# Kernel optimization log

Measured on AMD Instinct MI355X. Metric: run time of the kernel, lower is better.

Reference implementation:

```python
import jax, jax.numpy as jnp
import numpy as np
from jax import lax

D_MODEL = 1024
D_STATE = 16
BATCH = 4
SEQ = 2048
EPS = 1e-5


def setup_inputs() -> dict:
    key = jax.random.key(0)
    ks = jax.random.split(key, 5)
    x = jax.random.normal(ks[0], (BATCH, SEQ, D_MODEL), dtype=jnp.float32)
    A_log = jax.random.normal(ks[1], (D_MODEL, D_STATE), dtype=jnp.float32) * 0.1
    # nn.Linear default init ~ U(-1/sqrt(fan_in), 1/sqrt(fan_in))
    B_w = jax.random.uniform(ks[2], (D_STATE, D_MODEL), minval=-1.0, maxval=1.0) / np.sqrt(D_MODEL)
    C_w = jax.random.uniform(ks[3], (D_MODEL, D_STATE), minval=-1.0, maxval=1.0) / np.sqrt(D_STATE)
    D = jnp.ones((D_MODEL,), dtype=jnp.float32)
    gamma = jnp.ones((D_MODEL,), dtype=jnp.float32)
    beta = jnp.zeros((D_MODEL,), dtype=jnp.float32)
    return {"x": x, "A_log": A_log, "B_w": B_w, "C_w": C_w, "D": D, "gamma": gamma, "beta": beta}


def _layernorm(y, gamma, beta):
    mu = jnp.mean(y, axis=-1, keepdims=True)
    var = jnp.mean((y - mu) ** 2, axis=-1, keepdims=True)
    return (y - mu) * lax.rsqrt(var + EPS) * gamma + beta


def reference(x, A_log, B_w, C_w, D, gamma, beta):
    batch, seq_len, d = x.shape
    decay = jnp.exp(-jnp.exp(A_log))  # (d_model, d_state), exp(A) with A = -exp(A_log)
    # Precompute all B projections: (batch, seq, d_state)
    bx = jnp.einsum('bsd,nd->bsn', x, B_w)
    bx_t = jnp.swapaxes(bx, 0, 1)  # (seq, batch, d_state)

    def step(h, b_t):
        # h: (batch, d_model, d_state); b_t broadcast over d_model dim
        h = h * decay + b_t[:, None, :]
        return h, h.mean(axis=1)  # carry, per-step mean (batch, d_state)

    h0 = jnp.zeros((batch, d, A_log.shape[1]), dtype=x.dtype)
    _, hmeans = lax.scan(step, h0, bx_t)  # hmeans: (seq, batch, d_state)

    y = jnp.einsum('sbn,dn->bsd', hmeans, C_w) + D * x  # (batch, seq, d_model)
    return _layernorm(y, gamma, beta)
```

## Files before the change

kernel.cpp:

```cpp
#include <hip/hip_runtime.h>
#include <hip/hip_bf16.h>

#define D_MODEL 1024
#define D_STATE 16
#define BATCH   4
#define SEQ     2048
#define ROWS    (BATCH*SEQ)
#define WIN     64

#define K1_ROWS 8
__global__ __launch_bounds__(256, 4) void k_proj(const float* __restrict__ x,
                                                 const float* __restrict__ Bw,
                                                 const float* __restrict__ A_log,
                                                 float* __restrict__ bx,
                                                 float* __restrict__ KbarT) {
    __shared__ float xs[K1_ROWS][1024];
    __shared__ float red[4][8][K1_ROWS][2];
    const int tid = threadIdx.x;

    if (blockIdx.x >= ROWS / K1_ROWS) {
        const int n = blockIdx.x - ROWS / K1_ROWS;
        float* l2   = &xs[0][0];
        float* kred = &xs[1][0];
        const int delta = tid & 63;
        const int c     = tid >> 6;
        for (int d = tid; d < D_MODEL; d += 256) {
            float a = A_log[d * D_STATE + n];
            l2[d] = -expf(a) * 1.4426950408889634f;
        }
        __syncthreads();
        const float fdelta = (float)delta;
        float acc = 0.f;
        const int d0 = c * 256;
        for (int d = d0; d < d0 + 256; ++d)
            acc += exp2f(fdelta * l2[d]);
        kred[c * WIN + delta] = acc;
        __syncthreads();
        if (tid < WIN)
            KbarT[tid * D_STATE + n] =
                (kred[tid] + kred[WIN + tid] + kred[2 * WIN + tid] + kred[3 * WIN + tid])
                * (1.0f / 1024.0f);
        return;
    }

    const int np   = tid & 7;
    const int dblk = tid >> 3;
    const int row0 = blockIdx.x * K1_ROWS;
    const int lane = tid & 63, wid = tid >> 6;

    float4 bw0[8], bw1[8];
    {
        const float4* p0 = reinterpret_cast<const float4*>(Bw + (size_t)(2 * np    ) * 1024 + dblk * 32);
        const float4* p1 = reinterpret_cast<const float4*>(Bw + (size_t)(2 * np + 1) * 1024 + dblk * 32);
#pragma unroll
        for (int j = 0; j < 8; ++j) { bw0[j] = p0[j]; bw1[j] = p1[j]; }
    }

    const int chunk = tid >> 3;
    const int slotw = ((tid & 7) + chunk) & 7;
#pragma unroll
    for (int r = 0; r < K1_ROWS; ++r) {
        float4 v = reinterpret_cast<const float4*>(x + (size_t)(row0 + r) * 1024)[tid];
        *reinterpret_cast<float4*>(&xs[r][chunk * 32 + slotw * 4]) = v;
    }
    __syncthreads();

    float a0[K1_ROWS], a1[K1_ROWS];
#pragma unroll
    for (int r = 0; r < K1_ROWS; ++r) { a0[r] = 0.f; a1[r] = 0.f; }

#pragma unroll
    for (int r = 0; r < K1_ROWS; ++r) {
#pragma unroll
        for (int j = 0; j < 8; ++j) {
            const int slot = (j + dblk) & 7;
            float4 xv = *reinterpret_cast<const float4*>(&xs[r][dblk * 32 + slot * 4]);
            a0[r] = fmaf(xv.x, bw0[j].x, a0[r]); a0[r] = fmaf(xv.y, bw0[j].y, a0[r]);
            a0[r] = fmaf(xv.z, bw0[j].z, a0[r]); a0[r] = fmaf(xv.w, bw0[j].w, a0[r]);
            a1[r] = fmaf(xv.x, bw1[j].x, a1[r]); a1[r] = fmaf(xv.y, bw1[j].y, a1[r]);
            a1[r] = fmaf(xv.z, bw1[j].z, a1[r]); a1[r] = fmaf(xv.w, bw1[j].w, a1[r]);
        }
    }

#pragma unroll
    for (int r = 0; r < K1_ROWS; ++r) {
        float v0 = a0[r], v1 = a1[r];
        v0 += __shfl_xor(v0, 8);  v1 += __shfl_xor(v1, 8);
        v0 += __shfl_xor(v0, 16); v1 += __shfl_xor(v1, 16);
        v0 += __shfl_xor(v0, 32); v1 += __shfl_xor(v1, 32);
        a0[r] = v0; a1[r] = v1;
    }
    if (lane < 8) {
#pragma unroll
        for (int r = 0; r < K1_ROWS; ++r) {
            red[wid][lane][r][0] = a0[r];
            red[wid][lane][r][1] = a1[r];
        }
    }
    __syncthreads();
    if (tid < K1_ROWS * 16) {
        const int r = tid >> 4, n = tid & 15;
        float v = red[0][n >> 1][r][n & 1] + red[1][n >> 1][r][n & 1]
                + red[2][n >> 1][r][n & 1] + red[3][n >> 1][r][n & 1];
        bx[(size_t)(row0 + r) * D_STATE + n] = v;
    }
}

#define KO_ROWS 8
__global__ __launch_bounds__(256, 4) void k_tail(const float* __restrict__ x,
                                                 const float* __restrict__ bxg,
                                                 const float* __restrict__ KbarT,
                                                 const float* __restrict__ Cw,
                                                 const float* __restrict__ Dp,
                                                 const float* __restrict__ gamma,
                                                 const float* __restrict__ beta,
                                                 float* __restrict__ out) {
    const int tid = threadIdx.x;
    const int row0 = blockIdx.x * KO_ROWS;
    const int lane = tid & 63, wid = tid >> 6;
    __shared__ float4 bwin[71][4];
    __shared__ float4 kb4[WIN][4];
    __shared__ float4 hm4[KO_ROWS][4];
    __shared__ float red_s[2][4][4], red_q[2][4][4];

    kb4[tid >> 2][tid & 3] = reinterpret_cast<const float4*>(KbarT)[tid];
    const float4* bx4 = reinterpret_cast<const float4*>(bxg);
    for (int f = tid; f < 71 * 4; f += 256) {
        const int j = f >> 2, q = f & 3;
        long g = (long)row0 - 63 + j;
        if (g < 0) g = 0;
        bwin[j][q] = bx4[g * 4 + q];
    }
    __syncthreads();

    {
        const int r_f = tid >> 5, dc = (tid >> 2) & 7, nq = tid & 3;
        const int t0 = row0 & (SEQ - 1);
        float4 acc = {0.f, 0.f, 0.f, 0.f};
        if (t0 >= WIN) {
#pragma unroll
            for (int j = 0; j < 8; ++j) {
                const int delta = dc * 8 + j;
                const float4 b = bwin[63 + r_f - delta][nq];
                const float4 k = kb4[delta][nq];
                acc.x = fmaf(k.x, b.x, acc.x); acc.y = fmaf(k.y, b.y, acc.y);
                acc.z = fmaf(k.z, b.z, acc.z); acc.w = fmaf(k.w, b.w, acc.w);
            }
        } else {
            const int t = t0 + r_f;
#pragma unroll
            for (int j = 0; j < 8; ++j) {
                const int delta = dc * 8 + j;
                if (delta <= t) {
                    const float4 b = bwin[63 + r_f - delta][nq];
                    const float4 k = kb4[delta][nq];
                    acc.x = fmaf(k.x, b.x, acc.x); acc.y = fmaf(k.y, b.y, acc.y);
                    acc.z = fmaf(k.z, b.z, acc.z); acc.w = fmaf(k.w, b.w, acc.w);
                }
            }
        }
#pragma unroll
        for (int off = 4; off <= 16; off <<= 1) {
            acc.x += __shfl_xor(acc.x, off);
            acc.y += __shfl_xor(acc.y, off);
            acc.z += __shfl_xor(acc.z, off);
            acc.w += __shfl_xor(acc.w, off);
        }
        if (dc == 0) hm4[r_f][nq] = acc;
    }
    __syncthreads();

    float4 cw[4][4];
#pragma unroll
    for (int j = 0; j < 4; ++j) {
        const float4* p = reinterpret_cast<const float4*>(Cw + (size_t)(tid * 4 + j) * D_STATE);
#pragma unroll
        for (int q = 0; q < 4; ++q) cw[j][q] = p[q];
    }
    const float4 Dq = reinterpret_cast<const float4*>(Dp)[tid];
    const float4 gq = reinterpret_cast<const float4*>(gamma)[tid];
    const float4 bq = reinterpret_cast<const float4*>(beta)[tid];

    for (int h = 0; h < 2; ++h) {
        float4 y[4];
#pragma unroll
        for (int rr = 0; rr < 4; ++rr) {
            const int r = h * 4 + rr;
            const size_t row = row0 + r;
            const float4 h0 = hm4[r][0], h1 = hm4[r][1], h2 = hm4[r][2], h3 = hm4[r][3];
            const float4 xq = reinterpret_cast<const float4*>(x + row * D_MODEL)[tid];

            float4 v;
#pragma unroll
            for (int j = 0; j < 4; ++j) {
                float a = 0.f;
                a = fmaf(h0.x, cw[j][0].x, a); a = fmaf(h0.y, cw[j][0].y, a);
                a = fmaf(h0.z, cw[j][0].z, a); a = fmaf(h0.w, cw[j][0].w, a);
                a = fmaf(h1.x, cw[j][1].x, a); a = fmaf(h1.y, cw[j][1].y, a);
                a = fmaf(h1.z, cw[j][1].z, a); a = fmaf(h1.w, cw[j][1].w, a);
                a = fmaf(h2.x, cw[j][2].x, a); a = fmaf(h2.y, cw[j][2].y, a);
                a = fmaf(h2.z, cw[j][2].z, a); a = fmaf(h2.w, cw[j][2].w, a);
                a = fmaf(h3.x, cw[j][3].x, a); a = fmaf(h3.y, cw[j][3].y, a);
                a = fmaf(h3.z, cw[j][3].z, a); a = fmaf(h3.w, cw[j][3].w, a);
                ((float*)&v)[j] = a;
            }
            v.x = fmaf(Dq.x, xq.x, v.x);
            v.y = fmaf(Dq.y, xq.y, v.y);
            v.z = fmaf(Dq.z, xq.z, v.z);
            v.w = fmaf(Dq.w, xq.w, v.w);
            y[rr] = v;

            float s  = v.x + v.y + v.z + v.w;
            float sq = v.x*v.x + v.y*v.y + v.z*v.z + v.w*v.w;
            s += __shfl_xor(s, 1);  sq += __shfl_xor(sq, 1);
            s += __shfl_xor(s, 2);  sq += __shfl_xor(sq, 2);
            s += __shfl_xor(s, 4);  sq += __shfl_xor(sq, 4);
            s += __shfl_xor(s, 8);  sq += __shfl_xor(sq, 8);
            s += __shfl_xor(s, 16); sq += __shfl_xor(sq, 16);
            s += __shfl_xor(s, 32); sq += __shfl_xor(sq, 32);
            if (lane == 0) { red_s[h][rr][wid] = s; red_q[h][rr][wid] = sq; }
        }
        __syncthreads();

#pragma unroll
        for (int rr = 0; rr < 4; ++rr) {
            const int r = h * 4 + rr;
            const size_t row = row0 + r;
            const float ssum = red_s[h][rr][0] + red_s[h][rr][1] + red_s[h][rr][2] + red_s[h][rr][3];
            const float ssq  = red_q[h][rr][0] + red_q[h][rr][1] + red_q[h][rr][2] + red_q[h][rr][3];
            const float mu   = ssum * (1.0f / 1024.0f);
            const float var  = ssq * (1.0f / 1024.0f) - mu * mu;
            const float inv  = rsqrtf(var + 1e-5f);
            const float4 v = y[rr];
            float4 o;
            o.x = fmaf((v.x - mu) * inv, gq.x, bq.x);
            o.y = fmaf((v.y - mu) * inv, gq.y, bq.y);
            o.z = fmaf((v.z - mu) * inv, gq.z, bq.z);
            o.w = fmaf((v.w - mu) * inv, gq.w, bq.w);
            reinterpret_cast<float4*>(out + row * D_MODEL)[tid] = o;
        }
    }
}

extern "C" void kernel_launch(void* const* d_in, const int* in_sizes, int n_in,
                              void* d_out, int out_size, void* d_ws, size_t ws_size,
                              hipStream_t stream) {
    (void)in_sizes; (void)n_in; (void)out_size; (void)ws_size;
    const float* x     = (const float*)d_in[0];
    const float* A_log = (const float*)d_in[1];
    const float* B_w   = (const float*)d_in[2];
    const float* C_w   = (const float*)d_in[3];
    const float* Dp    = (const float*)d_in[4];
    const float* gamma = (const float*)d_in[5];
    const float* beta  = (const float*)d_in[6];
    float* out = (float*)d_out;

    float* bx = (float*)d_ws;
    float* kb = bx + (size_t)ROWS * D_STATE;

    k_proj<<<ROWS / K1_ROWS + D_STATE, 256, 0, stream>>>(x, B_w, A_log, bx, kb);
    k_tail<<<ROWS / KO_ROWS,           256, 0, stream>>>(x, bx, kb, C_w, Dp, gamma, beta, out);
}
```

Before: 56.83 us.

## Prefetch x rows early in tail kernel and schedule decay blocks first

The tail kernel now issues all eight x-row loads at kernel start, so their latency overlaps the bx window staging and the hidden-mean computation. The two half-row passes are merged into one pass with a single barrier. Launch bounds drop to 3 waves per SIMD to make room for the extra registers. In the projection kernel the 16 decay-kernel blocks move to the front of the grid so the long exp-sum blocks start first instead of trailing at the end.

```diff
diff --git a/kernel.cpp b/kernel.cpp
--- a/kernel.cpp
+++ b/kernel.cpp
@@ -18,8 +18,8 @@
     __shared__ float red[4][8][K1_ROWS][2];
     const int tid = threadIdx.x;
 
-    if (blockIdx.x >= ROWS / K1_ROWS) {
-        const int n = blockIdx.x - ROWS / K1_ROWS;
+    if (blockIdx.x < D_STATE) {
+        const int n = blockIdx.x;
         float* l2   = &xs[0][0];
         float* kred = &xs[1][0];
         const int delta = tid & 63;
@@ -45,7 +45,7 @@
 
     const int np   = tid & 7;
     const int dblk = tid >> 3;
-    const int row0 = blockIdx.x * K1_ROWS;
+    const int row0 = (blockIdx.x - D_STATE) * K1_ROWS;
     const int lane = tid & 63, wid = tid >> 6;
 
     float4 bw0[8], bw1[8];
@@ -107,7 +107,7 @@
 }
 
 #define KO_ROWS 8
-__global__ __launch_bounds__(256, 4) void k_tail(const float* __restrict__ x,
+__global__ __launch_bounds__(256, 3) void k_tail(const float* __restrict__ x,
                                                  const float* __restrict__ bxg,
                                                  const float* __restrict__ KbarT,
                                                  const float* __restrict__ Cw,
@@ -121,7 +121,12 @@
     __shared__ float4 bwin[71][4];
     __shared__ float4 kb4[WIN][4];
     __shared__ float4 hm4[KO_ROWS][4];
-    __shared__ float red_s[2][4][4], red_q[2][4][4];
+    __shared__ float red_s[KO_ROWS][4], red_q[KO_ROWS][4];
+
+    float4 xq[KO_ROWS];
+#pragma unroll
+    for (int r = 0; r < KO_ROWS; ++r)
+        xq[r] = reinterpret_cast<const float4*>(x + (size_t)(row0 + r) * D_MODEL)[tid];
 
     kb4[tid >> 2][tid & 3] = reinterpret_cast<const float4*>(KbarT)[tid];
     const float4* bx4 = reinterpret_cast<const float4*>(bxg);
@@ -181,64 +186,57 @@
     const float4 gq = reinterpret_cast<const float4*>(gamma)[tid];
     const float4 bq = reinterpret_cast<const float4*>(beta)[tid];
 
-    for (int h = 0; h < 2; ++h) {
-        float4 y[4];
-#pragma unroll
-        for (int rr = 0; rr < 4; ++rr) {
-            const int r = h * 4 + rr;
-            const size_t row = row0 + r;
-            const float4 h0 = hm4[r][0], h1 = hm4[r][1], h2 = hm4[r][2], h3 = hm4[r][3];
-            const float4 xq = reinterpret_cast<const float4*>(x + row * D_MODEL)[tid];
-
-            float4 v;
-#pragma unroll
-            for (int j = 0; j < 4; ++j) {
-                float a = 0.f;
-                a = fmaf(h0.x, cw[j][0].x, a); a = fmaf(h0.y, cw[j][0].y, a);
-                a = fmaf(h0.z, cw[j][0].z, a); a = fmaf(h0.w, cw[j][0].w, a);
-                a = fmaf(h1.x, cw[j][1].x, a); a = fmaf(h1.y, cw[j][1].y, a);
-                a = fmaf(h1.z, cw[j][1].z, a); a = fmaf(h1.w, cw[j][1].w, a);
-                a = fmaf(h2.x, cw[j][2].x, a); a = fmaf(h2.y, cw[j][2].y, a);
-                a = fmaf(h2.z, cw[j][2].z, a); a = fmaf(h2.w, cw[j][2].w, a);
-                a = fmaf(h3.x, cw[j][3].x, a); a = fmaf(h3.y, cw[j][3].y, a);
-                a = fmaf(h3.z, cw[j][3].z, a); a = fmaf(h3.w, cw[j][3].w, a);
-                ((float*)&v)[j] = a;
-            }
-            v.x = fmaf(Dq.x, xq.x, v.x);
-            v.y = fmaf(Dq.y, xq.y, v.y);
-            v.z = fmaf(Dq.z, xq.z, v.z);
-            v.w = fmaf(Dq.w, xq.w, v.w);
-            y[rr] = v;
-
-            float s  = v.x + v.y + v.z + v.w;
-            float sq = v.x*v.x + v.y*v.y + v.z*v.z + v.w*v.w;
-            s += __shfl_xor(s, 1);  sq += __shfl_xor(sq, 1);
-            s += __shfl_xor(s, 2);  sq += __shfl_xor(sq, 2);
-            s += __shfl_xor(s, 4);  sq += __shfl_xor(sq, 4);
-            s += __shfl_xor(s, 8);  sq += __shfl_xor(sq, 8);
-            s += __shfl_xor(s, 16); sq += __shfl_xor(sq, 16);
-            s += __shfl_xor(s, 32); sq += __shfl_xor(sq, 32);
-            if (lane == 0) { red_s[h][rr][wid] = s; red_q[h][rr][wid] = sq; }
-        }
-        __syncthreads();
-
-#pragma unroll
-        for (int rr = 0; rr < 4; ++rr) {
-            const int r = h * 4 + rr;
-            const size_t row = row0 + r;
-            const float ssum = red_s[h][rr][0] + red_s[h][rr][1] + red_s[h][rr][2] + red_s[h][rr][3];
-            const float ssq  = red_q[h][rr][0] + red_q[h][rr][1] + red_q[h][rr][2] + red_q[h][rr][3];
-            const float mu   = ssum * (1.0f / 1024.0f);
-            const float var  = ssq * (1.0f / 1024.0f) - mu * mu;
-            const float inv  = rsqrtf(var + 1e-5f);
-            const float4 v = y[rr];
-            float4 o;
-            o.x = fmaf((v.x - mu) * inv, gq.x, bq.x);
-            o.y = fmaf((v.y - mu) * inv, gq.y, bq.y);
-            o.z = fmaf((v.z - mu) * inv, gq.z, bq.z);
-            o.w = fmaf((v.w - mu) * inv, gq.w, bq.w);
-            reinterpret_cast<float4*>(out + row * D_MODEL)[tid] = o;
-        }
+    float4 y[KO_ROWS];
+#pragma unroll
+    for (int r = 0; r < KO_ROWS; ++r) {
+        const float4 h0 = hm4[r][0], h1 = hm4[r][1], h2 = hm4[r][2], h3 = hm4[r][3];
+        float4 v;
+#pragma unroll
+        for (int j = 0; j < 4; ++j) {
+            float a = 0.f;
+            a = fmaf(h0.x, cw[j][0].x, a); a = fmaf(h0.y, cw[j][0].y, a);
+            a = fmaf(h0.z, cw[j][0].z, a); a = fmaf(h0.w, cw[j][0].w, a);
+            a = fmaf(h1.x, cw[j][1].x, a); a = fmaf(h1.y, cw[j][1].y, a);
+            a = fmaf(h1.z, cw[j][1].z, a); a = fmaf(h1.w, cw[j][1].w, a);
+            a = fmaf(h2.x, cw[j][2].x, a); a = fmaf(h2.y, cw[j][2].y, a);
+            a = fmaf(h2.z, cw[j][2].z, a); a = fmaf(h2.w, cw[j][2].w, a);
+            a = fmaf(h3.x, cw[j][3].x, a); a = fmaf(h3.y, cw[j][3].y, a);
+            a = fmaf(h3.z, cw[j][3].z, a); a = fmaf(h3.w, cw[j][3].w, a);
+            ((float*)&v)[j] = a;
+        }
+        v.x = fmaf(Dq.x, xq[r].x, v.x);
+        v.y = fmaf(Dq.y, xq[r].y, v.y);
+        v.z = fmaf(Dq.z, xq[r].z, v.z);
+        v.w = fmaf(Dq.w, xq[r].w, v.w);
+        y[r] = v;
+
+        float s  = v.x + v.y + v.z + v.w;
+        float sq = v.x*v.x + v.y*v.y + v.z*v.z + v.w*v.w;
+        s += __shfl_xor(s, 1);  sq += __shfl_xor(sq, 1);
+        s += __shfl_xor(s, 2);  sq += __shfl_xor(sq, 2);
+        s += __shfl_xor(s, 4);  sq += __shfl_xor(sq, 4);
+        s += __shfl_xor(s, 8);  sq += __shfl_xor(sq, 8);
+        s += __shfl_xor(s, 16); sq += __shfl_xor(sq, 16);
+        s += __shfl_xor(s, 32); sq += __shfl_xor(sq, 32);
+        if (lane == 0) { red_s[r][wid] = s; red_q[r][wid] = sq; }
+    }
+    __syncthreads();
+
+#pragma unroll
+    for (int r = 0; r < KO_ROWS; ++r) {
+        const size_t row = row0 + r;
+        const float ssum = red_s[r][0] + red_s[r][1] + red_s[r][2] + red_s[r][3];
+        const float ssq  = red_q[r][0] + red_q[r][1] + red_q[r][2] + red_q[r][3];
+        const float mu   = ssum * (1.0f / 1024.0f);
+        const float var  = ssq * (1.0f / 1024.0f) - mu * mu;
+        const float inv  = rsqrtf(var + 1e-5f);
+        const float4 v = y[r];
+        float4 o;
+        o.x = fmaf((v.x - mu) * inv, gq.x, bq.x);
+        o.y = fmaf((v.y - mu) * inv, gq.y, bq.y);
+        o.z = fmaf((v.z - mu) * inv, gq.z, bq.z);
+        o.w = fmaf((v.w - mu) * inv, gq.w, bq.w);
+        reinterpret_cast<float4*>(out + row * D_MODEL)[tid] = o;
     }
 }
 
```

After: 49.10 us. 13.6% less time.
